# Optimization experiments

Measured on AMD Instinct MI355X. Metric: run time of the kernel, lower is better.

## Reference

```python
import jax, jax.numpy as jnp
import numpy as np
import math

NHEADS = 4


def _mab(Q, K, qw, qb, kw, kb, vw, vb, ow, ob, mask):
    """MAB2 from tripletformer: multi-head attention (head split via cat(split,0)),
    softmax scale uses sqrt(FULL dim_V), masked_fill(mask==0, -1e10), residual on
    the projected Q, then O + relu(fc_o(O))."""
    dv = qw.shape[1]
    dh = dv // NHEADS
    B, Nq, _ = Q.shape
    Nk = K.shape[1]
    Qh = (Q @ qw + qb).reshape(B, Nq, NHEADS, dh).transpose(0, 2, 1, 3)  # B,h,Nq,dh
    Kh = (K @ kw + kb).reshape(B, Nk, NHEADS, dh).transpose(0, 2, 1, 3)
    Vh = (K @ vw + vb).reshape(B, Nk, NHEADS, dh).transpose(0, 2, 1, 3)
    att = jnp.einsum('bhqd,bhkd->bhqk', Qh, Kh) * (1.0 / math.sqrt(dv))
    att = jnp.where(mask, att, jnp.asarray(-1e10, att.dtype))
    A = jax.nn.softmax(att, axis=-1)
    Oh = Qh + jnp.einsum('bhqk,bhkd->bhqd', A, Vh)
    O = Oh.transpose(0, 2, 1, 3).reshape(B, Nq, dv)
    return O + jax.nn.relu(O @ ow + ob)


def _forward(context_x, value, mask, obs_len, iff_w, iff_b, ind_points,
             q0w, q0b, k0w, k0b, v0w, v0b, o0w, o0b,
             q1w, q1b, k1w, k1b, v1w, v1b, o1w, o1b):
    B, L = context_x.shape
    D = value.shape[-1]
    mflat = mask.reshape(B, L * D)
    # stable stream compaction: observed entries first, original (time-major,
    # channel-minor) order preserved; truncate to static obs_len
    order = jnp.argsort(-mflat, axis=-1, stable=True)[:, :obs_len]  # (B, N)
    T = jnp.broadcast_to(context_x[:, :, None], (B, L, D)).reshape(B, L * D)
    C = jnp.broadcast_to(jnp.arange(D, dtype=jnp.int32), (B, L, D)).reshape(B, L * D)
    U = value.reshape(B, L * D)
    take = lambda a: jnp.take_along_axis(a, order, axis=-1)
    T_, U_, mk_ = take(T), take(U), take(mflat)
    Ch = jax.nn.one_hot(take(C), D, dtype=value.dtype)  # one_hot(num_classes=dim-2)
    X = jnp.concatenate([Ch, T_[..., None], U_[..., None]], axis=-1) * mk_[..., None]
    Y = jax.nn.relu(X @ iff_w + iff_b) * mk_[..., None]
    key_valid = mk_ > 0                        # (B, N)
    mask1 = key_valid[:, None, None, :]        # mab0: mask padded keys
    mask2 = key_valid[:, None, :, None]        # mab1: mask padded query rows
    Z = Y
    n_layers = ind_points.shape[0]
    for i in range(n_layers):
        I = jnp.broadcast_to(ind_points[i], (B,) + ind_points[i].shape)
        H = _mab(I, Z, q0w[i], q0b[i], k0w[i], k0b[i], v0w[i], v0b[i], o0w[i], o0b[i], mask1)
        Zn = _mab(Z, H, q1w[i], q1b[i], k1w[i], k1b[i], v1w[i], v1b[i], o1w[i], o1b[i], mask2)
        Z = Zn * mk_[..., None] + Z
    return Z, mk_[..., None]


def setup_inputs() -> dict:
    B, L, D, OBS, DK, M, NL = 16, 512, 41, 4096, 128, 128, 3
    key = jax.random.key(0)
    ks = jax.random.split(key, 16)
    context_x = jnp.sort(jax.random.uniform(ks[0], (B, L), dtype=jnp.float32), axis=-1)
    value = jax.random.normal(ks[1], (B, L, D), dtype=jnp.float32)
    # exactly OBS observed entries per batch row -> static packed length
    r = jax.random.uniform(ks[2], (B, L * D))
    kth = jnp.sort(r, axis=-1)[:, OBS]
    mask = (r < kth[:, None]).astype(jnp.float32).reshape(B, L, D)

    def w(k, shape, fan):
        return jax.random.normal(k, shape, dtype=jnp.float32) / math.sqrt(fan)

    inp = dict(
        context_x=context_x, value=value, mask=mask, obs_len=OBS,
        iff_w=w(ks[3], (D + 2, DK), D + 2), iff_b=jnp.zeros((DK,), jnp.float32),
        ind_points=w(ks[4], (NL, M, DK), DK),
    )
    for j, n in enumerate(['q0', 'k0', 'v0', 'o0', 'q1', 'k1', 'v1', 'o1']):
        inp[n + 'w'] = w(ks[5 + j], (NL, DK, DK), DK)
        inp[n + 'b'] = jnp.zeros((NL, DK), jnp.float32)
    return inp


def reference(context_x, value, mask, obs_len, iff_w, iff_b, ind_points,
              q0w, q0b, k0w, k0b, v0w, v0b, o0w, o0b,
              q1w, q1b, k1w, k1b, v1w, v1b, o1w, o1b):
    return _forward(context_x, value, mask, obs_len, iff_w, iff_b, ind_points,
                    q0w, q0b, k0w, k0b, v0w, v0b, o0w, o0b,
                    q1w, q1b, k1w, k1b, v1w, v1b, o1w, o1b)
```

## Files before the change

kernel.cpp:

```cpp
#include <hip/hip_runtime.h>
#include <math.h>

#define NBATCH 16
#define SEQL   512
#define DIM    41
#define LDFLAT (SEQL*DIM)
#define OBS    4096
#define DK     128
#define NH     4
#define DH     32

typedef short bf16x8 __attribute__((ext_vector_type(8)));
typedef short short8v __attribute__((ext_vector_type(8)));
typedef float floatx4 __attribute__((ext_vector_type(4)));

__device__ __forceinline__ short f2bf(float f) {
  union { float f; unsigned u; } v;
  v.f = f;
  unsigned r = (v.u + 0x7fffu + ((v.u >> 16) & 1u)) >> 16;
  return (short)r;
}
__device__ __forceinline__ float bf2f(short s) {
  union { unsigned u; float f; } v;
  v.u = ((unsigned)(unsigned short)s) << 16;
  return v.f;
}


__device__ __forceinline__ int swz(int row, int col) {
  return row * 128 + ((((col >> 3) ^ row) & 15) << 3) + (col & 7);
}

typedef struct { int4 v[4]; } WStageH;
__device__ __forceinline__ void stage_load_h(WStageH& s,
                                             const short* __restrict__ Wh,
                                             int tid) {
#pragma unroll
  for (int k = 0; k < 4; k++)
    s.v[k] = *(const int4*)&Wh[(size_t)tid * 8 + (size_t)k * 2048];
}
__device__ __forceinline__ void stage_write_h(short* Wl, const WStageH& s,
                                              int tid) {
#pragma unroll
  for (int k = 0; k < 4; k++) {
    int i = tid * 8 + k * 2048;
    *(int4*)&Wl[swz(i >> 7, i & 127)] = s.v[k];
  }
}
typedef struct { int4 v[2]; } WStageF;
__device__ __forceinline__ void stage_load_f(WStageF& s,
                                             const short* __restrict__ W,
                                             int tid) {
#pragma unroll
  for (int k = 0; k < 2; k++)
    s.v[k] = *(const int4*)&W[(size_t)tid * 8 + (size_t)k * 8192];
}
__device__ __forceinline__ void stage_write_f(short* Wl, const WStageF& s,
                                              int tid) {
#pragma unroll
  for (int k = 0; k < 2; k++) {
    int i = tid * 8 + k * 8192;
    *(int4*)&Wl[swz(i >> 7, i & 127)] = s.v[k];
  }
}

__device__ __forceinline__ void gemm4_s(const short* Wl, const bf16x8 af[4],
                                        int lm, int quad, floatx4 acc[4]) {
#pragma unroll
  for (int nt = 0; nt < 4; nt++) acc[nt] = (floatx4){0.f, 0.f, 0.f, 0.f};
#pragma unroll
  for (int kc = 0; kc < 4; kc++) {
    bf16x8 a = af[kc];
#pragma unroll
    for (int nt = 0; nt < 4; nt++) {
      bf16x8 b = *(const bf16x8*)&Wl[swz(nt * 16 + lm, kc * 32 + quad * 8)];
      acc[nt] = __builtin_amdgcn_mfma_f32_16x16x32_bf16(a, b, acc[nt], 0, 0, 0);
    }
  }
}
__device__ __forceinline__ void gemm2_s(const short* Wl, const bf16x8 af[4],
                                        int colq, int lm, int quad,
                                        floatx4 acc[2]) {
#pragma unroll
  for (int nt = 0; nt < 2; nt++) acc[nt] = (floatx4){0.f, 0.f, 0.f, 0.f};
#pragma unroll
  for (int kc = 0; kc < 4; kc++) {
    bf16x8 a = af[kc];
#pragma unroll
    for (int nt = 0; nt < 2; nt++) {
      bf16x8 b = *(const bf16x8*)&Wl[swz(colq * 32 + nt * 16 + lm,
                                         kc * 32 + quad * 8)];
      acc[nt] = __builtin_amdgcn_mfma_f32_16x16x32_bf16(a, b, acc[nt], 0, 0, 0);
    }
  }
}
__device__ __forceinline__ void load_af_s(const short* Xl, int strip, int lm,
                                          int quad, bf16x8 af[4]) {
#pragma unroll
  for (int kc = 0; kc < 4; kc++)
    af[kc] = *(const bf16x8*)&Xl[swz(strip * 16 + lm, kc * 32 + quad * 8)];
}
__device__ __forceinline__ void store_sl4(short* Sl, const floatx4 acc[4],
                                          const float* __restrict__ bias,
                                          int wv, int lm, int quad,
                                          int colbase) {
#pragma unroll
  for (int nt = 0; nt < 4; nt++) {
    int col = colbase + nt * 16 + lm;
    float bn = bias[col];
#pragma unroll
    for (int r = 0; r < 4; r++)
      Sl[swz(wv * 16 + quad * 4 + r, col)] = f2bf(acc[nt][r] + bn);
  }
}
__device__ __forceinline__ void write_hs_s(const short* Sl,
                                           short* __restrict__ out, int rb,
                                           int nshift, int tid) {
  int rr = tid >> 2, hh = tid & 3;
  int r = rb + rr;
  int bb = r >> nshift, nn = r & ((1 << nshift) - 1);
  size_t o = (((size_t)(bb * NH + hh) << nshift) + nn) * 32;
#pragma unroll
  for (int j = 0; j < 4; j++)
    *(int4*)&out[o + j * 8] = *(int4*)&Sl[swz(rr, hh * 32 + j * 8)];
}
__device__ __forceinline__ void write_hs_q(const short* Sl,
                                           short* __restrict__ out, int rb,
                                           int nshift, int strip, int colq,
                                           int lane) {
  int rr = strip * 16 + (lane >> 2);
  int r = rb + rr;
  int bb = r >> nshift, nn = r & ((1 << nshift) - 1);
  size_t o = (((size_t)(bb * NH + colq) << nshift) + nn) * 32 + (lane & 3) * 8;
  *(int4*)&out[o] = *(const int4*)&Sl[swz(rr, colq * 32 + (lane & 3) * 8)];
}

__global__ __launch_bounds__(1024) void prep_build_kernel(
    const float* __restrict__ q0w, const float* __restrict__ k0w,
    const float* __restrict__ v0w, const float* __restrict__ o0w,
    const float* __restrict__ q1w, const float* __restrict__ k1w,
    const float* __restrict__ v1w, const float* __restrict__ o1w,
    short* __restrict__ Wt,
    const float* __restrict__ mask, int* __restrict__ order,
    float* __restrict__ mk_out, float* __restrict__ mk_out2) {
  __shared__ float Tl[128 * 132];
  __shared__ int wsums[16];
  __shared__ int s_total_ones;
  __shared__ int s_chunk_ones;
  __shared__ int s_ones_base;
  __shared__ int s_zeros_base;
  int tid = threadIdx.x;

  if (blockIdx.x < 24) {
    int id = blockIdx.x, l = id >> 3, wi = id & 7;
    const float* s;
    switch (wi) {
      case 0: s = q0w; break; case 1: s = k0w; break;
      case 2: s = v0w; break; case 3: s = o0w; break;
      case 4: s = q1w; break; case 5: s = k1w; break;
      case 6: s = v1w; break; default: s = o1w; break;
    }
    s += (size_t)l * 16384;
    for (int i = tid * 4; i < 16384; i += 4096) {
      int k = i >> 7, n = i & 127;
      float4 x = *(const float4*)&s[i];
      Tl[k * 132 + n + 0] = x.x; Tl[k * 132 + n + 1] = x.y;
      Tl[k * 132 + n + 2] = x.z; Tl[k * 132 + n + 3] = x.w;
    }
    __syncthreads();
    short* dst = Wt + (size_t)id * 16384;
    int n = tid >> 3, k0 = (tid & 7) * 16;
    for (int jc = 0; jc < 2; jc++) {
      short8v t;
#pragma unroll
      for (int j = 0; j < 8; j++) t[j] = f2bf(Tl[(k0 + jc * 8 + j) * 132 + n]);
      *(short8v*)&dst[n * 128 + k0 + jc * 8] = t;
    }
    return;
  }

  int b = blockIdx.x - 24;
  const float* m = mask + (size_t)b * LDFLAT;
  int lane = tid & 63, w = tid >> 6;

  int cnt = 0;
  for (int j = tid; j < LDFLAT; j += 1024) cnt += (m[j] > 0.f) ? 1 : 0;
  for (int off = 32; off > 0; off >>= 1) cnt += __shfl_xor(cnt, off);
  if (lane == 0) wsums[w] = cnt;
  __syncthreads();
  if (tid == 0) {
    int t = 0;
    for (int i = 0; i < 16; i++) t += wsums[i];
    s_total_ones = t; s_ones_base = 0; s_zeros_base = 0;
  }
  __syncthreads();
  int total_ones = s_total_ones;

  for (int c0 = 0; c0 < LDFLAT; c0 += 1024) {
    __syncthreads();
    int j = c0 + tid;
    bool valid = (j < LDFLAT);
    float mv = valid ? m[j] : 0.f;
    int one = (valid && mv > 0.f) ? 1 : 0;
    int v = one;
    for (int off = 1; off < 64; off <<= 1) {
      int t = __shfl_up(v, (unsigned)off);
      if (lane >= off) v += t;
    }
    if (lane == 63) wsums[w] = v;
    __syncthreads();
    if (tid == 0) {
      int run = 0;
      for (int i = 0; i < 16; i++) { int t = wsums[i]; wsums[i] = run; run += t; }
      s_chunk_ones = run;
    }
    __syncthreads();
    int ones_before = (v - one) + wsums[w];
    int ob = s_ones_base, zb = s_zeros_base, chunk_ones = s_chunk_ones;
    int rem = LDFLAT - c0;
    int chunk_valid = rem < 1024 ? rem : 1024;
    int valid_before = tid < rem ? tid : rem;
    if (valid) {
      int pos = one ? (ob + ones_before)
                    : (total_ones + zb + (valid_before - ones_before));
      if (pos < OBS) {
        order[b * OBS + pos] = j;
        mk_out[b * OBS + pos] = mv;
        mk_out2[b * OBS + pos] = mv;
      }
    }
    __syncthreads();
    if (tid == 0) {
      s_ones_base = ob + chunk_ones;
      s_zeros_base = zb + (chunk_valid - chunk_ones);
    }
  }
}

__global__ __launch_bounds__(256, 3) void fusedA_kernel(
    const int* __restrict__ order, const float* __restrict__ mk_g,
    const float* __restrict__ cx, const float* __restrict__ value,
    const float* __restrict__ iff_w, const float* __restrict__ iff_b,
    float* __restrict__ Z,
    const short* __restrict__ Wk, const float* __restrict__ kbias,
    short* __restrict__ Kb,
    const short* __restrict__ Wv, const float* __restrict__ vbias,
    short* __restrict__ Vb,
    const short* __restrict__ Wq, const float* __restrict__ qbias,
    short* __restrict__ Qb,
    const float* __restrict__ indp, const short* __restrict__ WtAll,
    const float* __restrict__ q0b_all, short* __restrict__ qh_b) {
  __shared__ __align__(16) short Xl[64 * 128];
  __shared__ __align__(16) short WlA[64 * 128];
  __shared__ __align__(16) short WlB[64 * 128];
  int tid = threadIdx.x;
  int wv = tid >> 6, lane = tid & 63, lm = lane & 15, quad = lane >> 4;
  int r_l = lane >> 2, seg = lane & 3;
  int lrow = wv * 16 + r_l;

  if (blockIdx.x >= 1024) {
    int id = blockIdx.x - 1024;
    int l = id >> 1, rbq = (id & 1) * 64;
    const float* X = indp + (size_t)l * 16384 + (size_t)rbq * 128;
    const short* W = WtAll + (size_t)(l * 8) * 16384;
    const float* bias = q0b_all + (size_t)l * 128;
    short* out = qh_b + (size_t)l * 16384;
    WStageH sA, sB;
    stage_load_h(sA, W, tid);
    stage_load_h(sB, W + 8192, tid);
    const float* Xr = X + (size_t)lrow * 128;
#pragma unroll
    for (int jj = 0; jj < 8; jj++) {
      int col = seg * 32 + jj * 4;
      float4 x = *(const float4*)&Xr[col];
      *(short4*)&Xl[swz(lrow, col)] =
          make_short4(f2bf(x.x), f2bf(x.y), f2bf(x.z), f2bf(x.w));
    }
    stage_write_h(WlA, sA, tid);
    stage_write_h(WlB, sB, tid);
    __syncthreads();
    bf16x8 af[4];
    load_af_s(Xl, wv, lm, quad, af);
    floatx4 acc[4];
    gemm4_s(WlA, af, lm, quad, acc);
    store_sl4(Xl, acc, bias, wv, lm, quad, 0);
    gemm4_s(WlB, af, lm, quad, acc);
    store_sl4(Xl, acc, bias, wv, lm, quad, 64);
    write_hs_s(Xl, out, rbq, 7, tid);
    return;
  }

  int rb = blockIdx.x * 64;
  WStageH s0; stage_load_h(s0, Wk, tid);
  int grow = rb + lrow;
  int bb = grow >> 12;
  int j = order[grow];
  int l = j / DIM, d = j - l * DIM;
  float t = cx[bb * SEQL + l];
  float u = value[(size_t)bb * LDFLAT + j];
  float mkv = mk_g[grow];
#pragma unroll
  for (int jj = 0; jj < 8; jj++) {
    int col = seg * 32 + jj * 4;
    float4 w0 = *(const float4*)&iff_w[d * DK + col];
    float4 w1 = *(const float4*)&iff_w[41 * DK + col];
    float4 w2 = *(const float4*)&iff_w[42 * DK + col];
    float4 b4 = *(const float4*)&iff_b[col];
    float4 z;
    z.x = fmaxf(w0.x + t * w1.x + u * w2.x + b4.x, 0.f) * mkv;
    z.y = fmaxf(w0.y + t * w1.y + u * w2.y + b4.y, 0.f) * mkv;
    z.z = fmaxf(w0.z + t * w1.z + u * w2.z + b4.z, 0.f) * mkv;
    z.w = fmaxf(w0.w + t * w1.w + u * w2.w + b4.w, 0.f) * mkv;
    *(float4*)&Z[(size_t)grow * DK + col] = z;
    *(short4*)&Xl[swz(lrow, col)] =
        make_short4(f2bf(z.x), f2bf(z.y), f2bf(z.z), f2bf(z.w));
  }
  stage_write_h(WlA, s0, tid);
  __syncthreads();
  WStageH s1; stage_load_h(s1, Wk + 8192, tid);
  bf16x8 af[4];
  load_af_s(Xl, wv, lm, quad, af);
  floatx4 acc[4];
  gemm4_s(WlA, af, lm, quad, acc);
  store_sl4(Xl, acc, kbias, wv, lm, quad, 0);
  stage_write_h(WlB, s1, tid);
  __syncthreads();
  WStageH s2; stage_load_h(s2, Wv, tid);
  gemm4_s(WlB, af, lm, quad, acc);
  store_sl4(Xl, acc, kbias, wv, lm, quad, 64);
  write_hs_s(Xl, Kb, rb, 12, tid);
  stage_write_h(WlA, s2, tid);
  __syncthreads();
  WStageH s3; stage_load_h(s3, Wv + 8192, tid);
  gemm4_s(WlA, af, lm, quad, acc);
  store_sl4(Xl, acc, vbias, wv, lm, quad, 0);
  stage_write_h(WlB, s3, tid);
  __syncthreads();
  WStageH s4; stage_load_h(s4, Wq, tid);
  gemm4_s(WlB, af, lm, quad, acc);
  store_sl4(Xl, acc, vbias, wv, lm, quad, 64);
  write_hs_s(Xl, Vb, rb, 12, tid);
  stage_write_h(WlA, s4, tid);
  __syncthreads();
  WStageH s5; stage_load_h(s5, Wq + 8192, tid);
  gemm4_s(WlA, af, lm, quad, acc);
  store_sl4(Xl, acc, qbias, wv, lm, quad, 0);
  stage_write_h(WlB, s5, tid);
  __syncthreads();
  gemm4_s(WlB, af, lm, quad, acc);
  store_sl4(Xl, acc, qbias, wv, lm, quad, 64);
  write_hs_s(Xl, Qb, rb, 12, tid);
}

__global__ __launch_bounds__(256) void attn1_kernel(
    const short* __restrict__ Qh,
    const short* __restrict__ Kh, const short* __restrict__ Vh,
    const float* __restrict__ mk,
    float* __restrict__ Opart, float* __restrict__ mpart,
    float* __restrict__ lpart) {
  __shared__ __align__(16) short Ql[128 * 40];
  __shared__ __align__(16) short Kc[64 * 40];
  __shared__ __align__(16) short Vtc[32 * 74];
  __shared__ __align__(16) short Pl[128 * 72];
  __shared__ float mkc[64];
  int bh = blockIdx.x;
  int b = bh >> 2, h = bh & 3;
  int ks = blockIdx.y;
  int tid = threadIdx.x;
  int wv = tid >> 6, lane = tid & 63, lm = lane & 15, quad = lane >> 4;

  const float scale = 0.08838834764831845f;
  const short* kbase = Kh + ((size_t)bh * OBS + ks * 512) * 32;
  const short* vbase = Vh + ((size_t)bh * OBS + ks * 512) * 32;
  const float* mkb = mk + (size_t)b * OBS + ks * 512;

  int i0 = tid * 8;
  int r0 = i0 >> 5, cv = i0 & 31;
  int4 kreg = *(const int4*)&kbase[i0];
  int4 vreg = *(const int4*)&vbase[i0];
  float mreg = (tid < 64) ? mkb[tid] : 0.f;

  const short* qbg = Qh + (size_t)h * 128 * 32;
  for (int i = tid * 8; i < 128 * 32; i += 2048) {
    int r = i >> 5, c = i & 31;
    *(int4*)&Ql[r * 40 + c] = *(const int4*)&qbg[i];
  }
  __syncthreads();
  bf16x8 aq[2];
  aq[0] = *(bf16x8*)&Ql[(wv * 32 + lm) * 40 + quad * 8];
  aq[1] = *(bf16x8*)&Ql[(wv * 32 + 16 + lm) * 40 + quad * 8];

  float m_i[2][4], l_i[2][4];
  floatx4 oacc[2][2];
#pragma unroll
  for (int mt = 0; mt < 2; mt++) {
#pragma unroll
    for (int r = 0; r < 4; r++) { m_i[mt][r] = -1e30f; l_i[mt][r] = 0.f; }
    oacc[mt][0] = (floatx4){0.f, 0.f, 0.f, 0.f};
    oacc[mt][1] = (floatx4){0.f, 0.f, 0.f, 0.f};
  }

  for (int ch = 0; ch < 8; ch++) {
    __syncthreads();
    *(int4*)&Kc[r0 * 40 + cv] = kreg;
    {
      short* vv = (short*)&vreg;
#pragma unroll
      for (int j = 0; j < 8; j++) Vtc[(cv + j) * 74 + r0] = vv[j];
    }
    if (tid < 64) mkc[tid] = mreg;
    if (ch < 7) {
      kreg = *(const int4*)&kbase[(ch + 1) * 2048 + i0];
      vreg = *(const int4*)&vbase[(ch + 1) * 2048 + i0];
      if (tid < 64) mreg = mkb[(ch + 1) * 64 + tid];
    }
    __syncthreads();

    floatx4 sf[2][4];
#pragma unroll
    for (int nt = 0; nt < 4; nt++) {
      bf16x8 bfrag = *(bf16x8*)&Kc[(nt * 16 + lm) * 40 + quad * 8];
      floatx4 z = {0.f, 0.f, 0.f, 0.f};
      sf[0][nt] = __builtin_amdgcn_mfma_f32_16x16x32_bf16(aq[0], bfrag, z, 0, 0, 0);
      sf[1][nt] = __builtin_amdgcn_mfma_f32_16x16x32_bf16(aq[1], bfrag, z, 0, 0, 0);
    }
#pragma unroll
    for (int nt = 0; nt < 4; nt++) {
      float mkv = mkc[nt * 16 + lm];
      bool ok = mkv > 0.f;
#pragma unroll
      for (int mt = 0; mt < 2; mt++)
#pragma unroll
        for (int r = 0; r < 4; r++)
          sf[mt][nt][r] = ok ? sf[mt][nt][r] * scale : -1e10f;
    }
#pragma unroll
    for (int mt = 0; mt < 2; mt++) {
#pragma unroll
      for (int r = 0; r < 4; r++) {
        float mx = fmaxf(fmaxf(sf[mt][0][r], sf[mt][1][r]),
                         fmaxf(sf[mt][2][r], sf[mt][3][r]));
        mx = fmaxf(mx, __shfl_xor(mx, 1));
        mx = fmaxf(mx, __shfl_xor(mx, 2));
        mx = fmaxf(mx, __shfl_xor(mx, 4));
        mx = fmaxf(mx, __shfl_xor(mx, 8));
        float mn = fmaxf(m_i[mt][r], mx);
        float al = __expf(m_i[mt][r] - mn);
        float ps = 0.f;
#pragma unroll
        for (int nt = 0; nt < 4; nt++) {
          float p = __expf(sf[mt][nt][r] - mn);
          sf[mt][nt][r] = p;
          ps += p;
        }
        ps += __shfl_xor(ps, 1);
        ps += __shfl_xor(ps, 2);
        ps += __shfl_xor(ps, 4);
        ps += __shfl_xor(ps, 8);
        l_i[mt][r] = l_i[mt][r] * al + ps;
        m_i[mt][r] = mn;
        oacc[mt][0] *= al;
        oacc[mt][1] *= al;
      }
    }
#pragma unroll
    for (int mt = 0; mt < 2; mt++)
#pragma unroll
      for (int nt = 0; nt < 4; nt++)
#pragma unroll
        for (int r = 0; r < 4; r++)
          Pl[(wv * 32 + mt * 16 + quad * 4 + r) * 72 + nt * 16 + lm] =
              f2bf(sf[mt][nt][r]);
#pragma unroll
    for (int kc = 0; kc < 2; kc++) {
      bf16x8 vf0 = *(bf16x8*)&Vtc[lm * 74 + kc * 32 + quad * 8];
      bf16x8 vf1 = *(bf16x8*)&Vtc[(16 + lm) * 74 + kc * 32 + quad * 8];
#pragma unroll
      for (int mt = 0; mt < 2; mt++) {
        bf16x8 pf = *(bf16x8*)&Pl[(wv * 32 + mt * 16 + lm) * 72 + kc * 32 + quad * 8];
        oacc[mt][0] = __builtin_amdgcn_mfma_f32_16x16x32_bf16(pf, vf0, oacc[mt][0], 0, 0, 0);
        oacc[mt][1] = __builtin_amdgcn_mfma_f32_16x16x32_bf16(pf, vf1, oacc[mt][1], 0, 0, 0);
      }
    }
  }
  float* ob = Opart + (size_t)(ks * 64 + bh) * 128 * 32;
#pragma unroll
  for (int mt = 0; mt < 2; mt++) {
#pragma unroll
    for (int r = 0; r < 4; r++) {
      int row = wv * 32 + mt * 16 + quad * 4 + r;
      ob[(size_t)row * 32 + lm] = oacc[mt][0][r];
      ob[(size_t)row * 32 + 16 + lm] = oacc[mt][1][r];
      if (lm == 0) {
        mpart[(size_t)(ks * 64 + bh) * 128 + row] = m_i[mt][r];
        lpart[(size_t)(ks * 64 + bh) * 128 + row] = l_i[mt][r];
      }
    }
  }
}

__global__ __launch_bounds__(1024) void fusedB_kernel(
    const float* __restrict__ Opart, const float* __restrict__ mpart,
    const float* __restrict__ lpart, const short* __restrict__ qh,
    const short* __restrict__ Wo, const float* __restrict__ obias,
    const short* __restrict__ Wk, const float* __restrict__ kbias,
    const short* __restrict__ Wv, const float* __restrict__ vbias,
    short* __restrict__ khb, short* __restrict__ vhb) {
  __shared__ __align__(16) short Xl[64 * 128];
  __shared__ __align__(16) short WlA[128 * 128];
  __shared__ __align__(16) short WlB[128 * 128];
  int tid = threadIdx.x;
  int rb = blockIdx.x * 64;
  int b = rb >> 7, n0 = rb & 127;
  int wv = tid >> 6, lane = tid & 63, lm = lane & 15, quad = lane >> 4;
  int strip = wv & 3, colq = wv >> 2;
  WStageF sWo; stage_load_f(sWo, Wo, tid);
#pragma unroll
  for (int p = 0; p < 2; p++) {
    int slot = p * 1024 + tid;
    int pair = slot >> 3;
    int hh = pair & 3, rr = pair >> 2;
    int c4 = (slot & 7) * 4;
    int n = n0 + rr;
    int bh = b * 4 + hh;
    float mv[8], lv[8], m = -1e30f;
#pragma unroll
    for (int s = 0; s < 8; s++) {
      mv[s] = mpart[(size_t)(s * 64 + bh) * 128 + n];
      lv[s] = lpart[(size_t)(s * 64 + bh) * 128 + n];
      m = fmaxf(m, mv[s]);
    }
    float l = 0.f, oa0 = 0.f, oa1 = 0.f, oa2 = 0.f, oa3 = 0.f;
#pragma unroll
    for (int s = 0; s < 8; s++) {
      float w = __expf(mv[s] - m);
      l += lv[s] * w;
      float4 v = *(const float4*)&Opart[((size_t)(s * 64 + bh) * 128 + n) * 32 + c4];
      oa0 += v.x * w; oa1 += v.y * w; oa2 += v.z * w; oa3 += v.w * w;
    }
    float li = 1.f / l;
    int2 qi = *(const int2*)&qh[((size_t)hh * 128 + n) * 32 + c4];
    const short* qs = (const short*)&qi;
    short4 o4;
    o4.x = f2bf(bf2f(qs[0]) + oa0 * li);
    o4.y = f2bf(bf2f(qs[1]) + oa1 * li);
    o4.z = f2bf(bf2f(qs[2]) + oa2 * li);
    o4.w = f2bf(bf2f(qs[3]) + oa3 * li);
    *(short4*)&Xl[swz(rr, hh * 32 + c4)] = o4;
  }
  stage_write_f(WlA, sWo, tid);
  __syncthreads();
  bf16x8 afO[4];
  load_af_s(Xl, strip, lm, quad, afO);
  __syncthreads();
  WStageF sWk; stage_load_f(sWk, Wk, tid);
  floatx4 acc[2];
  gemm2_s(WlA, afO, colq, lm, quad, acc);
#pragma unroll
  for (int nt = 0; nt < 2; nt++) {
    int col = colq * 32 + nt * 16 + lm;
    float bn = obias[col];
#pragma unroll
    for (int r = 0; r < 4; r++) {
      int row = strip * 16 + quad * 4 + r;
      float ov = bf2f(Xl[swz(row, col)]);
      Xl[swz(row, col)] = f2bf(ov + fmaxf(acc[nt][r] + bn, 0.f));
    }
  }
  stage_write_f(WlB, sWk, tid);
  __syncthreads();
  bf16x8 afH[4];
  load_af_s(Xl, strip, lm, quad, afH);
  __syncthreads();
  WStageF sWv; stage_load_f(sWv, Wv, tid);
  gemm2_s(WlB, afH, colq, lm, quad, acc);
#pragma unroll
  for (int nt = 0; nt < 2; nt++) {
    int col = colq * 32 + nt * 16 + lm;
    float bn = kbias[col];
#pragma unroll
    for (int r = 0; r < 4; r++)
      Xl[swz(strip * 16 + quad * 4 + r, col)] = f2bf(acc[nt][r] + bn);
  }
  write_hs_q(Xl, khb, rb, 7, strip, colq, lane);
  stage_write_f(WlA, sWv, tid);
  __syncthreads();
  gemm2_s(WlA, afH, colq, lm, quad, acc);
#pragma unroll
  for (int nt = 0; nt < 2; nt++) {
    int col = colq * 32 + nt * 16 + lm;
    float bn = vbias[col];
#pragma unroll
    for (int r = 0; r < 4; r++)
      Xl[swz(strip * 16 + quad * 4 + r, col)] = f2bf(acc[nt][r] + bn);
  }
  write_hs_q(Xl, vhb, rb, 7, strip, colq, lane);
}

__global__ __launch_bounds__(256) void attn2_kernel(
    const short* __restrict__ Qh, const short* __restrict__ Kh,
    const short* __restrict__ Vh, short* __restrict__ O) {
  __shared__ __align__(16) short Kl[128 * 40];
  __shared__ __align__(16) short Vt[32 * 136];
  __shared__ __align__(16) short Ql[64 * 40];
  __shared__ __align__(16) short Pl[64 * 136];
  int bh = blockIdx.x;
  int b = bh >> 2, h = bh & 3;
  int q0 = blockIdx.y * 64;
  int tid = threadIdx.x;
  int wv = tid >> 6, lane = tid & 63, lm = lane & 15, quad = lane >> 4;
  const short* kb = Kh + (size_t)bh * 128 * 32;
  const short* vb = Vh + (size_t)bh * 128 * 32;
  const short* qb = Qh + ((size_t)bh * OBS + q0) * 32;

  for (int i = tid * 8; i < 128 * 32; i += 2048) {
    int r = i >> 5, c = i & 31;
    *(int4*)&Kl[r * 40 + c] = *(const int4*)&kb[i];
  }
  for (int i = tid * 8; i < 64 * 32; i += 2048) {
    int r = i >> 5, c = i & 31;
    *(int4*)&Ql[r * 40 + c] = *(const int4*)&qb[i];
  }
  for (int i = tid * 8; i < 128 * 32; i += 2048) {
    int r = i >> 5, c = i & 31;
    int4 vv4 = *(const int4*)&vb[i];
    short* vv = (short*)&vv4;
#pragma unroll
    for (int j = 0; j < 8; j++) Vt[(c + j) * 136 + r] = vv[j];
  }
  __syncthreads();

  const float scale = 0.08838834764831845f;
  bf16x8 afrag = *(bf16x8*)&Ql[(wv * 16 + lm) * 40 + quad * 8];
  floatx4 sf[8];
#pragma unroll
  for (int nt = 0; nt < 8; nt++) {
    bf16x8 bfrag = *(bf16x8*)&Kl[(nt * 16 + lm) * 40 + quad * 8];
    floatx4 z = {0.f, 0.f, 0.f, 0.f};
    sf[nt] = __builtin_amdgcn_mfma_f32_16x16x32_bf16(afrag, bfrag, z, 0, 0, 0);
  }
#pragma unroll
  for (int nt = 0; nt < 8; nt++) sf[nt] *= scale;
  float linv[4];
#pragma unroll
  for (int r = 0; r < 4; r++) {
    float mx = sf[0][r];
#pragma unroll
    for (int nt = 1; nt < 8; nt++) mx = fmaxf(mx, sf[nt][r]);
    mx = fmaxf(mx, __shfl_xor(mx, 1));
    mx = fmaxf(mx, __shfl_xor(mx, 2));
    mx = fmaxf(mx, __shfl_xor(mx, 4));
    mx = fmaxf(mx, __shfl_xor(mx, 8));
    float sum = 0.f;
#pragma unroll
    for (int nt = 0; nt < 8; nt++) {
      float p = __expf(sf[nt][r] - mx);
      sf[nt][r] = p;
      sum += p;
    }
    sum += __shfl_xor(sum, 1);
    sum += __shfl_xor(sum, 2);
    sum += __shfl_xor(sum, 4);
    sum += __shfl_xor(sum, 8);
    linv[r] = 1.f / sum;
  }
#pragma unroll
  for (int nt = 0; nt < 8; nt++)
#pragma unroll
    for (int r = 0; r < 4; r++)
      Pl[(wv * 16 + quad * 4 + r) * 136 + nt * 16 + lm] = f2bf(sf[nt][r]);

  floatx4 oacc[2] = {{0.f, 0.f, 0.f, 0.f}, {0.f, 0.f, 0.f, 0.f}};
#pragma unroll
  for (int kc = 0; kc < 4; kc++) {
    bf16x8 pf = *(bf16x8*)&Pl[(wv * 16 + lm) * 136 + kc * 32 + quad * 8];
#pragma unroll
    for (int nt2 = 0; nt2 < 2; nt2++) {
      bf16x8 vf = *(bf16x8*)&Vt[(nt2 * 16 + lm) * 136 + kc * 32 + quad * 8];
      oacc[nt2] = __builtin_amdgcn_mfma_f32_16x16x32_bf16(pf, vf, oacc[nt2], 0, 0, 0);
    }
  }
  short* Ol = Pl;
#pragma unroll
  for (int nt2 = 0; nt2 < 2; nt2++) {
#pragma unroll
    for (int r = 0; r < 4; r++) {
      int qrow = wv * 16 + quad * 4 + r;
      float q = bf2f(Ql[qrow * 40 + nt2 * 16 + lm]);
      Ol[qrow * 136 + nt2 * 16 + lm] = f2bf(q + oacc[nt2][r] * linv[r]);
    }
  }
  int rr = tid >> 2, seg = tid & 3;
  size_t o = ((size_t)b * OBS + q0 + rr) * 128 + h * 32 + seg * 8;
  *(int4*)&O[o] = *(int4*)&Ol[rr * 136 + seg * 8];
}

__global__ __launch_bounds__(256, 3) void fusedC_kernel(
    const short* __restrict__ Ob, const short* __restrict__ Wo,
    const float* __restrict__ obias, const float* __restrict__ mk,
    const float* __restrict__ Zin, float* __restrict__ Zout,
    const short* __restrict__ Wk, const float* __restrict__ kbias,
    short* __restrict__ Kb,
    const short* __restrict__ Wv, const float* __restrict__ vbias,
    short* __restrict__ Vb,
    const short* __restrict__ Wq, const float* __restrict__ qbias,
    short* __restrict__ Qb) {
  __shared__ __align__(16) short Xl[64 * 128];
  __shared__ __align__(16) short WlA[64 * 128];
  __shared__ __align__(16) short WlB[64 * 128];
  int tid = threadIdx.x;
  int rb = blockIdx.x * 64;
  int wv = tid >> 6, lane = tid & 63, lm = lane & 15, quad = lane >> 4;

  WStageH s0; stage_load_h(s0, Wo, tid);
  bf16x8 afO[4];
  {
    const short* arow = Ob + (size_t)(rb + wv * 16 + lm) * 128;
#pragma unroll
    for (int kc = 0; kc < 4; kc++) {
      afO[kc] = *(const bf16x8*)&arow[kc * 32 + quad * 8];
      *(bf16x8*)&Xl[swz(wv * 16 + lm, kc * 32 + quad * 8)] = afO[kc];
    }
  }
  int row0 = wv * 16 + quad * 4;
  float mkv[4];
#pragma unroll
  for (int r = 0; r < 4; r++) mkv[r] = mk[rb + row0 + r];
  stage_write_h(WlA, s0, tid);
  __syncthreads();
  WStageH s1; stage_load_h(s1, Wo + 8192, tid);
  floatx4 acc[4];
  gemm4_s(WlA, afO, lm, quad, acc);
#pragma unroll
  for (int nt = 0; nt < 4; nt++) {
    int col = nt * 16 + lm;
    float bn = obias[col];
#pragma unroll
    for (int r = 0; r < 4; r++) {
      int row = row0 + r;
      size_t g = (size_t)(rb + row) * 128 + col;
      float ov = bf2f(Xl[swz(row, col)]);
      float f = ov + fmaxf(acc[nt][r] + bn, 0.f);
      float zv = Zin[g] + f * mkv[r];
      Zout[g] = zv;
      Xl[swz(row, col)] = f2bf(zv);
    }
  }
  stage_write_h(WlB, s1, tid);
  __syncthreads();
  WStageH s2;
  if (Wk) stage_load_h(s2, Wk, tid);
  gemm4_s(WlB, afO, lm, quad, acc);
#pragma unroll
  for (int nt = 0; nt < 4; nt++) {
    int col = 64 + nt * 16 + lm;
    float bn = obias[col];
#pragma unroll
    for (int r = 0; r < 4; r++) {
      int row = row0 + r;
      size_t g = (size_t)(rb + row) * 128 + col;
      float ov = bf2f(Xl[swz(row, col)]);
      float f = ov + fmaxf(acc[nt][r] + bn, 0.f);
      float zv = Zin[g] + f * mkv[r];
      Zout[g] = zv;
      Xl[swz(row, col)] = f2bf(zv);
    }
  }
  if (Wk == nullptr) return;
  bf16x8 af[4];
  load_af_s(Xl, wv, lm, quad, af);
  stage_write_h(WlA, s2, tid);
  __syncthreads();
  WStageH s3; stage_load_h(s3, Wk + 8192, tid);
  gemm4_s(WlA, af, lm, quad, acc);
  store_sl4(Xl, acc, kbias, wv, lm, quad, 0);
  stage_write_h(WlB, s3, tid);
  __syncthreads();
  WStageH s4; stage_load_h(s4, Wv, tid);
  gemm4_s(WlB, af, lm, quad, acc);
  store_sl4(Xl, acc, kbias, wv, lm, quad, 64);
  write_hs_s(Xl, Kb, rb, 12, tid);
  stage_write_h(WlA, s4, tid);
  __syncthreads();
  WStageH s5; stage_load_h(s5, Wv + 8192, tid);
  gemm4_s(WlA, af, lm, quad, acc);
  store_sl4(Xl, acc, vbias, wv, lm, quad, 0);
  stage_write_h(WlB, s5, tid);
  __syncthreads();
  WStageH s6; stage_load_h(s6, Wq, tid);
  gemm4_s(WlB, af, lm, quad, acc);
  store_sl4(Xl, acc, vbias, wv, lm, quad, 64);
  write_hs_s(Xl, Vb, rb, 12, tid);
  stage_write_h(WlA, s6, tid);
  __syncthreads();
  WStageH s7; stage_load_h(s7, Wq + 8192, tid);
  gemm4_s(WlA, af, lm, quad, acc);
  store_sl4(Xl, acc, qbias, wv, lm, quad, 0);
  stage_write_h(WlB, s7, tid);
  __syncthreads();
  gemm4_s(WlB, af, lm, quad, acc);
  store_sl4(Xl, acc, qbias, wv, lm, quad, 64);
  write_hs_s(Xl, Qb, rb, 12, tid);
}

extern "C" void kernel_launch(void* const* d_in, const int* in_sizes, int n_in,
                              void* d_out, int out_size, void* d_ws,
                              size_t ws_size, hipStream_t stream) {
  const float* cx    = (const float*)d_in[0];
  const float* value = (const float*)d_in[1];
  const float* mask  = (const float*)d_in[2];
  const float* iff_w = (const float*)d_in[4];
  const float* iff_b = (const float*)d_in[5];
  const float* indp  = (const float*)d_in[6];
  const float* q0w = (const float*)d_in[7];  const float* q0b = (const float*)d_in[8];
  const float* k0w = (const float*)d_in[9];  const float* k0b = (const float*)d_in[10];
  const float* v0w = (const float*)d_in[11]; const float* v0b = (const float*)d_in[12];
  const float* o0w = (const float*)d_in[13]; const float* o0b = (const float*)d_in[14];
  const float* q1w = (const float*)d_in[15]; const float* q1b = (const float*)d_in[16];
  const float* k1w = (const float*)d_in[17]; const float* k1b = (const float*)d_in[18];
  const float* v1w = (const float*)d_in[19]; const float* v1b = (const float*)d_in[20];
  const float* o1w = (const float*)d_in[21]; const float* o1b = (const float*)d_in[22];

  char* ws = (char*)d_ws;
  short* Wt    = (short*)ws;  ws += (size_t)24 * 16384 * 2;
  int*   order = (int*)ws;    ws += (size_t)NBATCH * OBS * 4;
  float* mk_g  = (float*)ws;  ws += (size_t)NBATCH * OBS * 4;
  float* Z     = (float*)ws;  ws += (size_t)NBATCH * OBS * DK * 4;
  short* Qb    = (short*)ws;  ws += (size_t)NBATCH * OBS * DK * 2;
  short* Kb    = (short*)ws;  ws += (size_t)NBATCH * OBS * DK * 2;
  short* Vb    = (short*)ws;  ws += (size_t)NBATCH * OBS * DK * 2;
  short* Ob    = (short*)ws;  ws += (size_t)NBATCH * OBS * DK * 2;
  short* qh_b  = (short*)ws;  ws += (size_t)3 * 128 * DK * 2;
  short* khb   = (short*)ws;  ws += (size_t)NBATCH * NH * 128 * DH * 2;
  short* vhb   = (short*)ws;  ws += (size_t)NBATCH * NH * 128 * DH * 2;
  float* Opart = (float*)ws;  ws += (size_t)8 * 64 * 128 * 32 * 4;
  float* mpart = (float*)ws;  ws += (size_t)8 * 64 * 128 * 4;
  float* lpart = (float*)ws;  ws += (size_t)8 * 64 * 128 * 4;

  float* outZ  = (float*)d_out;
  float* outMk = outZ + (size_t)NBATCH * OBS * DK;

  prep_build_kernel<<<40, 1024, 0, stream>>>(q0w, k0w, v0w, o0w, q1w, k1w,
                                             v1w, o1w, Wt, mask, order, mk_g,
                                             outMk);

  const short* W[3][8];
  for (int l = 0; l < 3; l++)
    for (int wi = 0; wi < 8; wi++) W[l][wi] = Wt + (size_t)(l * 8 + wi) * 16384;

  fusedA_kernel<<<1030, 256, 0, stream>>>(
      order, mk_g, cx, value, iff_w, iff_b, Z,
      W[0][1], k0b, Kb, W[0][2], v0b, Vb, W[0][4], q1b, Qb,
      indp, Wt, q0b, qh_b);

  for (int l = 0; l < 3; l++) {
    attn1_kernel<<<dim3(64, 8), 256, 0, stream>>>(
        qh_b + (size_t)l * 16384, Kb, Vb, mk_g, Opart, mpart, lpart);
    fusedB_kernel<<<32, 1024, 0, stream>>>(
        Opart, mpart, lpart, qh_b + (size_t)l * 16384,
        W[l][3], o0b + (size_t)l * 128,
        W[l][5], k1b + (size_t)l * 128,
        W[l][6], v1b + (size_t)l * 128, khb, vhb);
    attn2_kernel<<<dim3(64, 64), 256, 0, stream>>>(Qb, khb, vhb, Ob);
    if (l < 2) {
      fusedC_kernel<<<1024, 256, 0, stream>>>(
          Ob, W[l][7], o1b + (size_t)l * 128, mk_g, Z, Z,
          W[l + 1][1], k0b + (size_t)(l + 1) * 128, Kb,
          W[l + 1][2], v0b + (size_t)(l + 1) * 128, Vb,
          W[l + 1][4], q1b + (size_t)(l + 1) * 128, Qb);
    } else {
      fusedC_kernel<<<1024, 256, 0, stream>>>(
          Ob, W[l][7], o1b + (size_t)l * 128, mk_g, Z, outZ,
          nullptr, nullptr, nullptr, nullptr, nullptr, nullptr,
          nullptr, nullptr, nullptr);
    }
  }
}
```

Measured before the change: 458.2 us.

## Stage bf16 weights into LDS with global_load_lds and pre-swizzled layout

Weight tiles were loaded into registers and then written to swizzled LDS. They are now copied straight from global memory into LDS with the global_load_lds builtin. To keep the swizzled layout the MFMA reads expect, the weight-transpose prep kernel now writes weights in swizzled order, so the linear direct-to-LDS copy lands correctly. This removes the register round trip and VGPR pressure, but it depends on the async copy finishing before the following __syncthreads and on the per-wave LDS offsets matching the swizzle.

```diff
diff --git a/kernel.cpp b/kernel.cpp
--- a/kernel.cpp
+++ b/kernel.cpp
@@ -31,37 +31,26 @@
   return row * 128 + ((((col >> 3) ^ row) & 15) << 3) + (col & 7);
 }
 
-typedef struct { int4 v[4]; } WStageH;
-__device__ __forceinline__ void stage_load_h(WStageH& s,
-                                             const short* __restrict__ Wh,
-                                             int tid) {
-#pragma unroll
-  for (int k = 0; k < 4; k++)
-    s.v[k] = *(const int4*)&Wh[(size_t)tid * 8 + (size_t)k * 2048];
-}
-__device__ __forceinline__ void stage_write_h(short* Wl, const WStageH& s,
-                                              int tid) {
-#pragma unroll
-  for (int k = 0; k < 4; k++) {
-    int i = tid * 8 + k * 2048;
-    *(int4*)&Wl[swz(i >> 7, i & 127)] = s.v[k];
-  }
-}
-typedef struct { int4 v[2]; } WStageF;
-__device__ __forceinline__ void stage_load_f(WStageF& s,
+__device__ __forceinline__ void glds16(const short* g, short* l) {
+  __builtin_amdgcn_global_load_lds(
+      (const __attribute__((address_space(1))) void*)g,
+      (__attribute__((address_space(3))) void*)l, 16, 0, 0);
+}
+__device__ __forceinline__ void stage_glds_h(short* Wl,
                                              const short* __restrict__ W,
                                              int tid) {
+  int wb = (tid >> 6) * 512;
+#pragma unroll
+  for (int k = 0; k < 4; k++)
+    glds16(&W[(size_t)tid * 8 + (size_t)k * 2048], &Wl[wb + k * 2048]);
+}
+__device__ __forceinline__ void stage_glds_f(short* Wl,
+                                             const short* __restrict__ W,
+                                             int tid) {
+  int wb = (tid >> 6) * 512;
 #pragma unroll
   for (int k = 0; k < 2; k++)
-    s.v[k] = *(const int4*)&W[(size_t)tid * 8 + (size_t)k * 8192];
-}
-__device__ __forceinline__ void stage_write_f(short* Wl, const WStageF& s,
-                                              int tid) {
-#pragma unroll
-  for (int k = 0; k < 2; k++) {
-    int i = tid * 8 + k * 8192;
-    *(int4*)&Wl[swz(i >> 7, i & 127)] = s.v[k];
-  }
+    glds16(&W[(size_t)tid * 8 + (size_t)k * 8192], &Wl[wb + k * 8192]);
 }
 
 __device__ __forceinline__ void gemm4_s(const short* Wl, const bf16x8 af[4],
@@ -174,7 +163,7 @@
       short8v t;
 #pragma unroll
       for (int j = 0; j < 8; j++) t[j] = f2bf(Tl[(k0 + jc * 8 + j) * 132 + n]);
-      *(short8v*)&dst[n * 128 + k0 + jc * 8] = t;
+      *(short8v*)&dst[swz(n, k0 + jc * 8)] = t;
     }
     return;
   }
@@ -265,9 +254,8 @@
     const short* W = WtAll + (size_t)(l * 8) * 16384;
     const float* bias = q0b_all + (size_t)l * 128;
     short* out = qh_b + (size_t)l * 16384;
-    WStageH sA, sB;
-    stage_load_h(sA, W, tid);
-    stage_load_h(sB, W + 8192, tid);
+    stage_glds_h(WlA, W, tid);
+    stage_glds_h(WlB, W + 8192, tid);
     const float* Xr = X + (size_t)lrow * 128;
 #pragma unroll
     for (int jj = 0; jj < 8; jj++) {
@@ -276,8 +264,6 @@
       *(short4*)&Xl[swz(lrow, col)] =
           make_short4(f2bf(x.x), f2bf(x.y), f2bf(x.z), f2bf(x.w));
     }
-    stage_write_h(WlA, sA, tid);
-    stage_write_h(WlB, sB, tid);
     __syncthreads();
     bf16x8 af[4];
     load_af_s(Xl, wv, lm, quad, af);
@@ -291,7 +277,7 @@
   }
 
   int rb = blockIdx.x * 64;
-  WStageH s0; stage_load_h(s0, Wk, tid);
+  stage_glds_h(WlA, Wk, tid);
   int grow = rb + lrow;
   int bb = grow >> 12;
   int j = order[grow];
@@ -315,37 +301,31 @@
     *(short4*)&Xl[swz(lrow, col)] =
         make_short4(f2bf(z.x), f2bf(z.y), f2bf(z.z), f2bf(z.w));
   }
-  stage_write_h(WlA, s0, tid);
-  __syncthreads();
-  WStageH s1; stage_load_h(s1, Wk + 8192, tid);
+  __syncthreads();
+  stage_glds_h(WlB, Wk + 8192, tid);
   bf16x8 af[4];
   load_af_s(Xl, wv, lm, quad, af);
   floatx4 acc[4];
   gemm4_s(WlA, af, lm, quad, acc);
   store_sl4(Xl, acc, kbias, wv, lm, quad, 0);
-  stage_write_h(WlB, s1, tid);
-  __syncthreads();
-  WStageH s2; stage_load_h(s2, Wv, tid);
+  __syncthreads();
+  stage_glds_h(WlA, Wv, tid);
   gemm4_s(WlB, af, lm, quad, acc);
   store_sl4(Xl, acc, kbias, wv, lm, quad, 64);
   write_hs_s(Xl, Kb, rb, 12, tid);
-  stage_write_h(WlA, s2, tid);
-  __syncthreads();
-  WStageH s3; stage_load_h(s3, Wv + 8192, tid);
+  __syncthreads();
+  stage_glds_h(WlB, Wv + 8192, tid);
   gemm4_s(WlA, af, lm, quad, acc);
   store_sl4(Xl, acc, vbias, wv, lm, quad, 0);
-  stage_write_h(WlB, s3, tid);
-  __syncthreads();
-  WStageH s4; stage_load_h(s4, Wq, tid);
+  __syncthreads();
+  stage_glds_h(WlA, Wq, tid);
   gemm4_s(WlB, af, lm, quad, acc);
   store_sl4(Xl, acc, vbias, wv, lm, quad, 64);
   write_hs_s(Xl, Vb, rb, 12, tid);
-  stage_write_h(WlA, s4, tid);
-  __syncthreads();
-  WStageH s5; stage_load_h(s5, Wq + 8192, tid);
+  __syncthreads();
+  stage_glds_h(WlB, Wq + 8192, tid);
   gemm4_s(WlA, af, lm, quad, acc);
   store_sl4(Xl, acc, qbias, wv, lm, quad, 0);
-  stage_write_h(WlB, s5, tid);
   __syncthreads();
   gemm4_s(WlB, af, lm, quad, acc);
   store_sl4(Xl, acc, qbias, wv, lm, quad, 64);
@@ -514,7 +494,7 @@
   int b = rb >> 7, n0 = rb & 127;
   int wv = tid >> 6, lane = tid & 63, lm = lane & 15, quad = lane >> 4;
   int strip = wv & 3, colq = wv >> 2;
-  WStageF sWo; stage_load_f(sWo, Wo, tid);
+  stage_glds_f(WlA, Wo, tid);
 #pragma unroll
   for (int p = 0; p < 2; p++) {
     int slot = p * 1024 + tid;
@@ -548,12 +528,11 @@
     o4.w = f2bf(bf2f(qs[3]) + oa3 * li);
     *(short4*)&Xl[swz(rr, hh * 32 + c4)] = o4;
   }
-  stage_write_f(WlA, sWo, tid);
   __syncthreads();
   bf16x8 afO[4];
   load_af_s(Xl, strip, lm, quad, afO);
   __syncthreads();
-  WStageF sWk; stage_load_f(sWk, Wk, tid);
+  stage_glds_f(WlB, Wk, tid);
   floatx4 acc[2];
   gemm2_s(WlA, afO, colq, lm, quad, acc);
 #pragma unroll
@@ -567,12 +546,11 @@
       Xl[swz(row, col)] = f2bf(ov + fmaxf(acc[nt][r] + bn, 0.f));
     }
   }
-  stage_write_f(WlB, sWk, tid);
   __syncthreads();
   bf16x8 afH[4];
   load_af_s(Xl, strip, lm, quad, afH);
   __syncthreads();
-  WStageF sWv; stage_load_f(sWv, Wv, tid);
+  stage_glds_f(WlA, Wv, tid);
   gemm2_s(WlB, afH, colq, lm, quad, acc);
 #pragma unroll
   for (int nt = 0; nt < 2; nt++) {
@@ -583,7 +561,6 @@
       Xl[swz(strip * 16 + quad * 4 + r, col)] = f2bf(acc[nt][r] + bn);
   }
   write_hs_q(Xl, khb, rb, 7, strip, colq, lane);
-  stage_write_f(WlA, sWv, tid);
   __syncthreads();
   gemm2_s(WlA, afH, colq, lm, quad, acc);
 #pragma unroll
@@ -712,7 +689,7 @@
   int rb = blockIdx.x * 64;
   int wv = tid >> 6, lane = tid & 63, lm = lane & 15, quad = lane >> 4;
 
-  WStageH s0; stage_load_h(s0, Wo, tid);
+  stage_glds_h(WlA, Wo, tid);
   bf16x8 afO[4];
   {
     const short* arow = Ob + (size_t)(rb + wv * 16 + lm) * 128;
@@ -726,9 +703,8 @@
   float mkv[4];
 #pragma unroll
   for (int r = 0; r < 4; r++) mkv[r] = mk[rb + row0 + r];
-  stage_write_h(WlA, s0, tid);
-  __syncthreads();
-  WStageH s1; stage_load_h(s1, Wo + 8192, tid);
+  __syncthreads();
+  stage_glds_h(WlB, Wo + 8192, tid);
   floatx4 acc[4];
   gemm4_s(WlA, afO, lm, quad, acc);
 #pragma unroll
@@ -746,10 +722,8 @@
       Xl[swz(row, col)] = f2bf(zv);
     }
   }
-  stage_write_h(WlB, s1, tid);
-  __syncthreads();
-  WStageH s2;
-  if (Wk) stage_load_h(s2, Wk, tid);
+  __syncthreads();
+  if (Wk) stage_glds_h(WlA, Wk, tid);
   gemm4_s(WlB, afO, lm, quad, acc);
 #pragma unroll
   for (int nt = 0; nt < 4; nt++) {
@@ -769,34 +743,28 @@
   if (Wk == nullptr) return;
   bf16x8 af[4];
   load_af_s(Xl, wv, lm, quad, af);
-  stage_write_h(WlA, s2, tid);
-  __syncthreads();
-  WStageH s3; stage_load_h(s3, Wk + 8192, tid);
+  __syncthreads();
+  stage_glds_h(WlB, Wk + 8192, tid);
   gemm4_s(WlA, af, lm, quad, acc);
   store_sl4(Xl, acc, kbias, wv, lm, quad, 0);
-  stage_write_h(WlB, s3, tid);
-  __syncthreads();
-  WStageH s4; stage_load_h(s4, Wv, tid);
+  __syncthreads();
+  stage_glds_h(WlA, Wv, tid);
   gemm4_s(WlB, af, lm, quad, acc);
   store_sl4(Xl, acc, kbias, wv, lm, quad, 64);
   write_hs_s(Xl, Kb, rb, 12, tid);
-  stage_write_h(WlA, s4, tid);
-  __syncthreads();
-  WStageH s5; stage_load_h(s5, Wv + 8192, tid);
+  __syncthreads();
+  stage_glds_h(WlB, Wv + 8192, tid);
   gemm4_s(WlA, af, lm, quad, acc);
   store_sl4(Xl, acc, vbias, wv, lm, quad, 0);
-  stage_write_h(WlB, s5, tid);
-  __syncthreads();
-  WStageH s6; stage_load_h(s6, Wq, tid);
+  __syncthreads();
+  stage_glds_h(WlA, Wq, tid);
   gemm4_s(WlB, af, lm, quad, acc);
   store_sl4(Xl, acc, vbias, wv, lm, quad, 64);
   write_hs_s(Xl, Vb, rb, 12, tid);
-  stage_write_h(WlA, s6, tid);
-  __syncthreads();
-  WStageH s7; stage_load_h(s7, Wq + 8192, tid);
+  __syncthreads();
+  stage_glds_h(WlB, Wq + 8192, tid);
   gemm4_s(WlA, af, lm, quad, acc);
   store_sl4(Xl, acc, qbias, wv, lm, quad, 0);
-  stage_write_h(WlB, s7, tid);
   __syncthreads();
   gemm4_s(WlB, af, lm, quad, acc);
   store_sl4(Xl, acc, qbias, wv, lm, quad, 64);
```

Result: faster. 445.3 us, median of 2 (-2.8%).
